# Kernel optimization log

Hardware: AMD Instinct MI355X
Metric: run time of the kernel (lower is better)

## Reference

```python
import jax, jax.numpy as jnp
import numpy as np

E = 256; H = 8; HD = E // H
L_LEN = 300; A_LEN = 250
T = 768; B = 4
NEG = -1e9


def setup_inputs() -> dict:
    rng = jax.random.key(0)
    ks = jax.random.split(rng, 16)
    n = lambda k, s, sc=1.0: jax.random.normal(k, s, dtype=jnp.float32) * sc
    return {
        "query": n(ks[0], (T, B, E)),
        "key": n(ks[1], (T, B, E)),
        "value": n(ks[2], (T, B, E)),
        "in_proj_w": n(ks[3], (3 * E, E), 0.05),
        "in_proj_b": jnp.zeros((3 * E,), jnp.float32),
        "out_w": n(ks[4], (7, E, E), 0.05),
        "out_b": jnp.zeros((7, E), jnp.float32),
        "s_l_w": n(ks[5], (E, 4 * E), 0.05),
        "s_l_b": jnp.zeros((E,), jnp.float32),
        "s_a_w": n(ks[6], (E, 4 * E), 0.05),
        "s_a_b": jnp.zeros((E,), jnp.float32),
        "s_v_w": n(ks[7], (E, 4 * E), 0.05),
        "s_v_b": jnp.zeros((E,), jnp.float32),
        "final_w": n(ks[8], (E, E), 0.05),
        "final_b": jnp.zeros((E,), jnp.float32),
    }


def _forward(query, key, value, in_proj_w, in_proj_b, out_w, out_b,
             s_l_w, s_l_b, s_a_w, s_a_b, s_v_w, s_v_b, final_w, final_b):
    t, b, e = query.shape
    scaling = HD ** -0.5
    Wq, Wk, Wv = in_proj_w[:E], in_proj_w[E:2 * E], in_proj_w[2 * E:]
    bq, bk, bv = in_proj_b[:E], in_proj_b[E:2 * E], in_proj_b[2 * E:]
    q = (query @ Wq.T + bq) * scaling
    k = key @ Wk.T + bk
    v = value @ Wv.T + bv
    # (T, B, E) -> (B*H, T, HD)
    sh = lambda x: x.reshape(t, b * H, HD).transpose(1, 0, 2)
    q, k, v = sh(q), sh(k), sh(v)
    # shared QK^T, reused by all 7 masked branches
    scores = jnp.einsum('bth,bsh->bts', q, k)  # (B*H, T, T)
    idx = jnp.arange(t)
    seg = jnp.where(idx < L_LEN, 0, jnp.where(idx < L_LEN + A_LEN, 1, 2))

    def branch(i, mods):
        # m[j] = 1 iff position j belongs to one of the selected modalities
        m = sum((seg == s) for s in mods).astype(scores.dtype)  # (T,)
        # additive mask: in-set query attends only in-set keys; out-of-set
        # query rows get all -1e9 (uniform softmax, zeroed by row mask below)
        add = jnp.where((m[:, None] * m[None, :]) > 0, 0.0, NEG)
        w = jax.nn.softmax(scores + add, axis=-1) * m[None, :, None]
        o = jnp.einsum('bts,bsh->bth', w, v * m[None, :, None])
        o = o.transpose(1, 0, 2).reshape(t, b, e)
        return o @ out_w[i].T + out_b[i]

    attn_lav = branch(0, (0, 1, 2))
    attn_la = branch(1, (0, 1))
    attn_lv = branch(2, (0, 2))
    attn_av = branch(3, (1, 2))
    attn_l = branch(4, (0,))
    attn_a = branch(5, (1,))
    attn_v = branch(6, (2,))

    sl = jnp.concatenate([attn_lav, attn_la, attn_lv, attn_l], -1) @ s_l_w.T + s_l_b
    sa = jnp.concatenate([attn_lav, attn_la, attn_av, attn_a], -1) @ s_a_w.T + s_a_b
    sv = jnp.concatenate([attn_lav, attn_lv, attn_av, attn_v], -1) @ s_v_w.T + s_v_b
    return (sl + sa + sv) @ final_w.T + final_b


def reference(query, key, value, in_proj_w, in_proj_b, out_w, out_b,
              s_l_w, s_l_b, s_a_w, s_a_b, s_v_w, s_v_b, final_w, final_b):
    return _forward(query, key, value, in_proj_w, in_proj_b, out_w, out_b,
                    s_l_w, s_l_b, s_a_w, s_a_b, s_v_w, s_v_b, final_w, final_b)
```

## Files before the change

### kernel.cpp

```cpp
#include <hip/hip_runtime.h>
#include <hip/hip_bf16.h>

#define E 256
#define H 8
#define HD 32
#define T 768
#define B 4
#define BH 32

typedef __attribute__((ext_vector_type(8))) short bf16x8;
typedef __attribute__((ext_vector_type(4))) float f32x4;
typedef __attribute__((ext_vector_type(16))) float f32x16;

__device__ __forceinline__ float b2f(__hip_bfloat16 x) { return __bfloat162float(x); }

__device__ __forceinline__ unsigned short f2bf_u(float x) {
    __hip_bfloat16 h = __float2bfloat16(x);
    return *(unsigned short*)&h;
}
__device__ __forceinline__ float bfu2f(unsigned short u) {
    return __uint_as_float(((unsigned int)u) << 16);
}

__device__ __forceinline__ int detect_f32(const void* query) {
    const unsigned short* q = (const unsigned short*)query;
    int lane = threadIdx.x & 63;
    int bad = 0;
    #pragma unroll
    for (int i = 0; i < 4; ++i) {
        float v = bfu2f(q[lane + i * 64]);
        bad |= (!(v == v) || fabsf(v) > 1e4f) ? 1 : 0;
    }
    return __any(bad) ? 1 : 0;
}

__device__ __forceinline__ void f8_split(const float* v, bf16x8& h, bf16x8& l) {
    #pragma unroll
    for (int e = 0; e < 8; ++e) {
        unsigned short hu = f2bf_u(v[e]);
        h[e] = (short)hu;
        l[e] = (short)f2bf_u(v[e] - bfu2f(hu));
    }
}

#define MFMA3(ACC, AH, AL, BH_, BL_)                                         \
    ACC = __builtin_amdgcn_mfma_f32_16x16x32_bf16(AH, BH_, ACC, 0, 0, 0);    \
    ACC = __builtin_amdgcn_mfma_f32_16x16x32_bf16(AH, BL_, ACC, 0, 0, 0);    \
    ACC = __builtin_amdgcn_mfma_f32_16x16x32_bf16(AL, BH_, ACC, 0, 0, 0);

#define MFMA3W(ACC, AH, AL, BH_, BL_)                                        \
    ACC = __builtin_amdgcn_mfma_f32_32x32x16_bf16(AH, BH_, ACC, 0, 0, 0);    \
    ACC = __builtin_amdgcn_mfma_f32_32x32x16_bf16(AH, BL_, ACC, 0, 0, 0);    \
    ACC = __builtin_amdgcn_mfma_f32_32x32x16_bf16(AL, BH_, ACC, 0, 0, 0);

__device__ __forceinline__ bf16x8 mk8(int a, int b, int c, int d) {
    union { int i[4]; bf16x8 v; } u;
    u.i[0] = a; u.i[1] = b; u.i[2] = c; u.i[3] = d;
    return u.v;
}

__device__ __forceinline__ float ldu(const void* p, size_t i, int f32) {
    if (f32) return ((const float*)p)[i];
    return b2f(((const __hip_bfloat16*)p)[i]);
}

__device__ __forceinline__ float gsum_load(int i, int r2, int r,
                                           const void* sl, const void* sa,
                                           const void* sv, int f32)
{
    size_t base = (size_t)r2 * 1024;
    switch (i) {
        case 0: return ldu(sl, base + r, f32) + ldu(sa, base + r, f32) + ldu(sv, base + r, f32);
        case 1: return ldu(sl, base + 256 + r, f32) + ldu(sa, base + 256 + r, f32);
        case 2: return ldu(sl, base + 512 + r, f32) + ldu(sv, base + 256 + r, f32);
        case 3: return ldu(sa, base + 512 + r, f32) + ldu(sv, base + 512 + r, f32);
        case 4: return ldu(sl, base + 768 + r, f32);
        case 5: return ldu(sa, base + 768 + r, f32);
        default: return ldu(sv, base + 768 + r, f32);
    }
}

__global__ __launch_bounds__(256) void stage1_kernel(
    const void* query, const void* key, const void* value, const void* w,
    const void* sl, const void* sa, const void* sv, const void* outw,
    const void* outb, const void* slb, const void* sab, const void* svb,
    unsigned short* __restrict__ XFh, unsigned short* __restrict__ XFl,
    unsigned short* __restrict__ WFh, unsigned short* __restrict__ WFl,
    unsigned short* __restrict__ GFh, unsigned short* __restrict__ GFl,
    unsigned short* __restrict__ OWFh, unsigned short* __restrict__ OWFl,
    float* __restrict__ c0)
{
    __shared__ float red[256];
    int f32 = detect_f32(query);
    if (blockIdx.x < 1696) {
        int item = blockIdx.x * 256 + threadIdx.x;
        if (item < 294912) {
            int inp = item / 98304;
            int rem = item % 98304;
            int row = rem >> 5, kg = rem & 31;
            const void* X = (inp == 0) ? query : (inp == 1) ? key : value;
            float v[8];
            if (f32) {
                const float4* p = (const float4*)((const float*)X +
                                   (size_t)row * 256 + kg * 8);
                *(float4*)&v[0] = p[0];
                *(float4*)&v[4] = p[1];
            } else {
                #pragma unroll
                for (int j = 0; j < 8; ++j)
                    v[j] = ldu(X, (size_t)row * 256 + kg * 8 + j, 0);
            }
            bf16x8 h, l;
            f8_split(v, h, l);
            int rb = row >> 4, kb = kg >> 2;
            int lane = (row & 15) | ((kg & 3) << 4);
            size_t idx = (((size_t)(inp * 192 + rb) * 8 + kb) * 64 + lane) * 8;
            *(bf16x8*)&XFh[idx] = h;
            *(bf16x8*)&XFl[idx] = l;
        } else if (item < 319488) {
            int rem = item - 294912;
            int gc = rem >> 5, kg = rem & 31;
            float v[8];
            if (f32) {
                const float4* p = (const float4*)((const float*)w +
                                   (size_t)gc * 256 + kg * 8);
                *(float4*)&v[0] = p[0];
                *(float4*)&v[4] = p[1];
            } else {
                #pragma unroll
                for (int j = 0; j < 8; ++j)
                    v[j] = ldu(w, (size_t)gc * 256 + kg * 8 + j, 0);
            }
            bf16x8 h, l;
            f8_split(v, h, l);
            int sec = gc >> 8, c = gc & 255;
            int cb = c >> 4, kb = kg >> 2;
            int lane = (c & 15) | ((kg & 3) << 4);
            size_t idx = (((size_t)(sec * 16 + cb) * 8 + kb) * 64 + lane) * 8;
            *(bf16x8*)&WFh[idx] = h;
            *(bf16x8*)&WFl[idx] = l;
        } else if (item < 376832) {
            int rem = item - 319488;
            int i = rem >> 13;
            int rest = rem & 8191;
            int r2 = rest >> 5, kg = rest & 31;
            float v[8];
            #pragma unroll
            for (int j = 0; j < 8; ++j)
                v[j] = gsum_load(i, r2, kg * 8 + j, sl, sa, sv, f32);
            bf16x8 h, l;
            f8_split(v, h, l);
            int rb = r2 >> 4, kb = kg >> 2;
            int lane = (r2 & 15) | ((kg & 3) << 4);
            size_t idx = (((size_t)(i * 16 + rb) * 8 + kb) * 64 + lane) * 8;
            *(bf16x8*)&GFh[idx] = h;
            *(bf16x8*)&GFl[idx] = l;
        } else if (item < 434176) {
            int rem = item - 376832;
            int i = rem >> 13;
            int rest = rem & 8191;
            int kg = rest >> 8, c = rest & 255;
            float v[8];
            #pragma unroll
            for (int j = 0; j < 8; ++j)
                v[j] = ldu(outw, (size_t)i * 65536 + (kg * 8 + j) * 256 + c, f32);
            bf16x8 h, l;
            f8_split(v, h, l);
            int cb = c >> 4, kb = kg >> 2;
            int lane = (c & 15) | ((kg & 3) << 4);
            size_t idx = (((size_t)(i * 16 + cb) * 8 + kb) * 64 + lane) * 8;
            *(bf16x8*)&OWFh[idx] = h;
            *(bf16x8*)&OWFl[idx] = l;
        }
    } else {
        int r2 = blockIdx.x - 1696, m = threadIdx.x;
        float acc = 0.f;
        #pragma unroll
        for (int i = 0; i < 7; ++i)
            acc += ldu(outb, i * 256 + m, f32) * gsum_load(i, r2, m, sl, sa, sv, f32);
        red[m] = acc;
        __syncthreads();
        for (int s = 128; s > 0; s >>= 1) {
            if (m < s) red[m] += red[m + s];
            __syncthreads();
        }
        if (m == 0)
            c0[r2] = red[0] + ldu(slb, r2, f32) + ldu(sab, r2, f32) + ldu(svb, r2, f32);
    }
}

__global__ __launch_bounds__(256) void stage2_kernel(
    const unsigned short* __restrict__ XFh, const unsigned short* __restrict__ XFl,
    const unsigned short* __restrict__ WFh, const unsigned short* __restrict__ WFl,
    const void* bias, const void* query,
    float* __restrict__ qws,
    unsigned short* __restrict__ KRh, unsigned short* __restrict__ KRl,
    unsigned short* __restrict__ VFh, unsigned short* __restrict__ VFl,
    const unsigned short* __restrict__ GFh, const unsigned short* __restrict__ GFl,
    const unsigned short* __restrict__ OWFh, const unsigned short* __restrict__ OWFl,
    float* __restrict__ Mtmp,
    const float* __restrict__ c0, const void* finalw, const void* finalb,
    float* __restrict__ d0)
{
    __shared__ float red[256];
    int bxx = blockIdx.x;
    if (bxx < 2304) {
        int f32 = detect_f32(query);
        int bx = bxx % 12;
        int rb = bxx / 12;
        int sec = bx >> 2, cg = bx & 3;
        int w = threadIdx.x >> 6, lane = threadIdx.x & 63;
        int m = lane & 15, quad = lane >> 4;
        int cb = cg * 4 + w;

        const unsigned short* Ah = XFh + (((size_t)(sec * 192 + rb) * 8) * 64 + lane) * 8;
        const unsigned short* Al = XFl + (((size_t)(sec * 192 + rb) * 8) * 64 + lane) * 8;
        const unsigned short* Bh = WFh + (((size_t)(sec * 16 + cb) * 8) * 64 + lane) * 8;
        const unsigned short* Bl = WFl + (((size_t)(sec * 16 + cb) * 8) * 64 + lane) * 8;

        f32x4 acc = {};
        #pragma unroll
        for (int kb = 0; kb < 8; ++kb) {
            size_t off = (size_t)kb * 512;
            bf16x8 ah = *(const bf16x8*)(Ah + off);
            bf16x8 al = *(const bf16x8*)(Al + off);
            bf16x8 bh = *(const bf16x8*)(Bh + off);
            bf16x8 bl = *(const bf16x8*)(Bl + off);
            MFMA3(acc, ah, al, bh, bl)
        }

        int c_local = cb * 16 + m;
        float bv = ldu(bias, sec * 256 + c_local, f32);
        int h = c_local >> 5, hd = c_local & 31;

        if (sec == 0) {
            #pragma unroll
            for (int rr = 0; rr < 4; ++rr) {
                int row = rb * 16 + quad * 4 + rr;
                int t = row >> 2, b = row & 3;
                float val = (acc[rr] + bv) * 0.17677669529663687f;
                qws[((size_t)((b * H + h) * T + t)) * HD + hd] = val;
            }
        } else if (sec == 1) {
            #pragma unroll
            for (int rr = 0; rr < 4; ++rr) {
                int row = rb * 16 + quad * 4 + rr;
                int s = row >> 2, b = row & 3;
                int bh_ = b * 8 + h;
                float val = acc[rr] + bv;
                unsigned short hu = f2bf_u(val);
                unsigned short lu = f2bf_u(val - bfu2f(hu));
                size_t bi = ((size_t)bh_ * 768 + s) * 32 + hd;
                KRh[bi] = hu;
                KRl[bi] = lu;
            }
        } else {
            #pragma unroll
            for (int rr = 0; rr < 4; ++rr) {
                int row = rb * 16 + quad * 4 + rr;
                int s = row >> 2, b = row & 3;
                int bh_ = b * 8 + h;
                float val = acc[rr] + bv;
                unsigned short hu = f2bf_u(val);
                unsigned short lu = f2bf_u(val - bfu2f(hu));
                int s16 = s >> 4, hp = (s >> 3) & 1, j = s & 7;
                size_t bi = (((size_t)bh_ * 48 + s16) * 64 + hp * 32 + hd) * 8 + j;
                VFh[bi] = hu;
                VFl[bi] = lu;
            }
        }
    } else if (bxx < 2752) {
        int idx = bxx - 2304;
        int cgrp = idx & 3;
        int rb   = (idx >> 2) & 15;
        int i    = idx >> 6;
        int w = threadIdx.x >> 6, lane = threadIdx.x & 63;
        int m = lane & 15, quad = lane >> 4;
        int cb = cgrp * 4 + w;

        const unsigned short* Ah = GFh + (((size_t)(i * 16 + rb) * 8) * 64 + lane) * 8;
        const unsigned short* Al = GFl + (((size_t)(i * 16 + rb) * 8) * 64 + lane) * 8;
        const unsigned short* Bh = OWFh + (((size_t)(i * 16 + cb) * 8) * 64 + lane) * 8;
        const unsigned short* Bl = OWFl + (((size_t)(i * 16 + cb) * 8) * 64 + lane) * 8;

        f32x4 acc = {};
        #pragma unroll
        for (int kb = 0; kb < 8; ++kb) {
            size_t off = (size_t)kb * 512;
            bf16x8 ah = *(const bf16x8*)(Ah + off);
            bf16x8 al = *(const bf16x8*)(Al + off);
            bf16x8 bh = *(const bf16x8*)(Bh + off);
            bf16x8 bl = *(const bf16x8*)(Bl + off);
            MFMA3(acc, ah, al, bh, bl)
        }
        #pragma unroll
        for (int rr = 0; rr < 4; ++rr) {
            int r2 = rb * 16 + quad * 4 + rr;
            Mtmp[(size_t)i * 65536 + r2 * 256 + cb * 16 + m] = acc[rr];
        }
    } else {
        int f32 = detect_f32(query);
        int e = bxx - 2752, r = threadIdx.x;
        red[r] = c0[r] * ldu(finalw, (size_t)e * 256 + r, f32);
        __syncthreads();
        for (int s = 128; s > 0; s >>= 1) {
            if (r < s) red[r] += red[r + s];
            __syncthreads();
        }
        if (r == 0)
            d0[e] = red[0] + ldu(finalb, e, f32);
    }
}

__global__ __launch_bounds__(256, 2) void stage3_kernel(
    const float* __restrict__ qws,
    const unsigned short* __restrict__ KRh, const unsigned short* __restrict__ KRl,
    const unsigned short* __restrict__ VFh, const unsigned short* __restrict__ VFl,
    unsigned short* __restrict__ Ohi, unsigned short* __restrict__ Olo,
    const float* __restrict__ Mtmp, const void* finalw, const void* query,
    unsigned short* __restrict__ DThi, unsigned short* __restrict__ DTlo)
{
    __shared__ __align__(16) float SMEM[7104];
    int tid = threadIdx.x;

    if (blockIdx.x < 768) {
        float (*AC2)[3][32][36] = (float(*)[3][32][36])&SMEM[0];
        float (*SS2)[3][32]     = (float(*)[3][32])&SMEM[6912];
        int tile = blockIdx.x % 24;
        int bh   = blockIdx.x / 24;
        int t0 = tile * 32;
        int w = tid >> 6, lane = tid & 63;
        int ln = lane & 31, h = lane >> 5;

        bf16x8 qbh[2], qbl[2];
        {
            const float* qr = qws + ((size_t)bh * T + t0 + ln) * HD + h * 8;
            #pragma unroll
            for (int c = 0; c < 2; ++c) {
                float qv[8];
                *(float4*)&qv[0] = *(const float4*)(qr + c * 16);
                *(float4*)&qv[4] = *(const float4*)(qr + c * 16 + 4);
                f8_split(qv, qbh[c], qbl[c]);
            }
        }

        f32x16 accA = {}, accB = {};
        float ssA = 0.f, ssB = 0.f;

        for (int q = 0; q < 3; ++q) {
            int ch = w * 3 + q;
            int sbase = ch * 64;
            int route = (ch == 5) ? 1 : (ch == 4 || ch == 8) ? 2 : 0;
            int bnd = (ch == 4) ? 300 : 550;
            bool c12 = (ch == 4);

            #pragma unroll
            for (int st = 0; st < 2; ++st) {
                size_t krow = ((size_t)bh * 768 + sbase + st * 32 + ln) * 32 + h * 8;
                bf16x8 kh0 = *(const bf16x8*)(KRh + krow);
                bf16x8 kl0 = *(const bf16x8*)(KRl + krow);
                bf16x8 kh1 = *(const bf16x8*)(KRh + krow + 16);
                bf16x8 kl1 = *(const bf16x8*)(KRl + krow + 16);
                f32x16 d = {};
                MFMA3W(d, kh0, kl0, qbh[0], qbl[0])
                MFMA3W(d, kh1, kl1, qbh[1], qbl[1])

                int PH[8], PL[8];
                #pragma unroll
                for (int p = 0; p < 8; ++p) {
                    float e0 = __expf(d[2 * p]);
                    float e1 = __expf(d[2 * p + 1]);
                    if (route == 2) {
                        int r0 = 2 * p;
                        int s0 = sbase + st * 32 + (r0 & 3) + 8 * (r0 >> 2) + 4 * h;
                        if (s0 < bnd) ssA += e0; else ssB += e0;
                        if (s0 + 1 < bnd) ssA += e1; else ssB += e1;
                    } else if (route == 1) { ssB += e0 + e1; }
                    else { ssA += e0 + e1; }
                    unsigned b0 = __float_as_uint(e0), b1 = __float_as_uint(e1);
                    float l0 = e0 - __uint_as_float(b0 & 0xffff0000u);
                    float l1 = e1 - __uint_as_float(b1 & 0xffff0000u);
                    PH[p] = (int)((b0 >> 16) | (b1 & 0xffff0000u));
                    PL[p] = (int)((__float_as_uint(l0) >> 16) |
                                  (__float_as_uint(l1) & 0xffff0000u));
                }

                #pragma unroll
                for (int ksl = 0; ksl < 2; ++ksl) {
                    int ks = st * 2 + ksl;
                    int cc = 4 * ksl;
                    size_t vidx = (((size_t)bh * 48 + ch * 4 + ks) * 64 + lane) * 8;
                    bf16x8 vbh = *(const bf16x8*)(VFh + vidx);
                    bf16x8 vbl = *(const bf16x8*)(VFl + vidx);

                    int sh0 = __shfl_xor(PH[cc+0], 32);
                    int sh1 = __shfl_xor(PH[cc+1], 32);
                    int sh2 = __shfl_xor(PH[cc+2], 32);
                    int sh3 = __shfl_xor(PH[cc+3], 32);
                    int sl0 = __shfl_xor(PL[cc+0], 32);
                    int sl1 = __shfl_xor(PL[cc+1], 32);
                    int sl2 = __shfl_xor(PL[cc+2], 32);
                    int sl3 = __shfl_xor(PL[cc+3], 32);
                    int FH0 = h ? sh2 : PH[cc+0];
                    int FH1 = h ? sh3 : PH[cc+1];
                    int FH2 = h ? PH[cc+2] : sh0;
                    int FH3 = h ? PH[cc+3] : sh1;
                    int FL0 = h ? sl2 : PL[cc+0];
                    int FL1 = h ? sl3 : PL[cc+1];
                    int FL2 = h ? PL[cc+2] : sl0;
                    int FL3 = h ? PL[cc+3] : sl1;
                    bf16x8 feh = mk8(FH0, FH1, FH2, FH3);
                    bf16x8 fel = mk8(FL0, FL1, FL2, FL3);

                    if (route == 0)      { MFMA3W(accA, feh, fel, vbh, vbl) }
                    else if (route == 1) { MFMA3W(accB, feh, fel, vbh, vbl) }
                    else {
                        if (ks < 2)       { MFMA3W(accA, feh, fel, vbh, vbl) }
                        else if (ks == 3) { MFMA3W(accB, feh, fel, vbh, vbl) }
                        else {
                            int a0 = h ? (c12 ? FH0 : 0) : FH0;
                            int a1 = h ? (c12 ? FH1 : 0) : FH1;
                            int a2 = h ? 0 : FH2;
                            int a3 = h ? 0 : (c12 ? FH3 : 0);
                            int b0 = h ? (c12 ? 0 : FH0) : 0;
                            int b1 = h ? (c12 ? 0 : FH1) : 0;
                            int b2 = h ? FH2 : 0;
                            int b3 = h ? FH3 : (c12 ? 0 : FH3);
                            int la0 = h ? (c12 ? FL0 : 0) : FL0;
                            int la1 = h ? (c12 ? FL1 : 0) : FL1;
                            int la2 = h ? 0 : FL2;
                            int la3 = h ? 0 : (c12 ? FL3 : 0);
                            int lb0 = h ? (c12 ? 0 : FL0) : 0;
                            int lb1 = h ? (c12 ? 0 : FL1) : 0;
                            int lb2 = h ? FL2 : 0;
                            int lb3 = h ? FL3 : (c12 ? 0 : FL3);
                            bf16x8 fha = mk8(a0, a1, a2, a3), fla = mk8(la0, la1, la2, la3);
                            bf16x8 fhb = mk8(b0, b1, b2, b3), flb = mk8(lb0, lb1, lb2, lb3);
                            MFMA3W(accA, fha, fla, vbh, vbl)
                            MFMA3W(accB, fhb, flb, vbh, vbl)
                        }
                    }
                }
            }
        }

        ssA += __shfl_xor(ssA, 32);
        ssB += __shfl_xor(ssB, 32);

        int bsel = w & 1;
        f32x16 zz = {};
        f32x16 o0 = (w <= 1) ? accA : zz;
        f32x16 o1 = (w == 1) ? accB : (w == 2) ? accA : zz;
        f32x16 o2 = (w == 2) ? accB : (w == 3) ? accA : zz;
        float s0 = (w <= 1) ? ssA : 0.f;
        float s1 = (w == 1) ? ssB : (w == 2) ? ssA : 0.f;
        float s2 = (w == 2) ? ssB : (w == 3) ? ssA : 0.f;

        if (w < 2) {
            #pragma unroll
            for (int r = 0; r < 16; ++r) {
                int t = (r & 3) + 8 * (r >> 2) + 4 * h;
                AC2[bsel][0][t][ln] = o0[r];
                AC2[bsel][1][t][ln] = o1[r];
                AC2[bsel][2][t][ln] = o2[r];
            }
            if (h == 0) {
                SS2[bsel][0][ln] = s0;
                SS2[bsel][1][ln] = s1;
                SS2[bsel][2][ln] = s2;
            }
        }
        __syncthreads();
        if (w >= 2) {
            #pragma unroll
            for (int r = 0; r < 16; ++r) {
                int t = (r & 3) + 8 * (r >> 2) + 4 * h;
                AC2[bsel][1][t][ln] += o1[r];
                AC2[bsel][2][t][ln] += o2[r];
            }
            if (h == 0) {
                SS2[bsel][1][ln] += s1;
                SS2[bsel][2][ln] += s2;
            }
        }
        __syncthreads();

        int tt = tid >> 3, q4 = tid & 7;
        float Pv[3][4], S[3];
        #pragma unroll
        for (int sg = 0; sg < 3; ++sg) {
            const float4 a = *(const float4*)&AC2[0][sg][tt][q4 * 4];
            const float4 b = *(const float4*)&AC2[1][sg][tt][q4 * 4];
            Pv[sg][0] = a.x + b.x; Pv[sg][1] = a.y + b.y;
            Pv[sg][2] = a.z + b.z; Pv[sg][3] = a.w + b.w;
            S[sg] = SS2[0][sg][tt] + SS2[1][sg][tt];
        }

        int t_glob = t0 + tt;
        int g = (t_glob < 300) ? 0 : (t_glob < 550 ? 1 : 2);
        int b_ = bh >> 3, h_ = bh & 7;
        int row = b_ * T + t_glob;
        int lslot = (row & 15) + ((q4 >> 1) << 4);
        int j0 = (q4 & 1) * 4;
        size_t fbase = (((size_t)(row >> 4) * 56 + h_) * 64 + lslot) * 8 + j0;
        const int masks[7] = {7, 3, 5, 6, 1, 2, 4};
        #pragma unroll
        for (int i = 0; i < 7; ++i) {
            int mm = masks[i];
            float n0 = 0.f, n1 = 0.f, n2 = 0.f, n3 = 0.f, den = 0.f;
            if (mm & 1) { n0 += Pv[0][0]; n1 += Pv[0][1]; n2 += Pv[0][2]; n3 += Pv[0][3]; den += S[0]; }
            if (mm & 2) { n0 += Pv[1][0]; n1 += Pv[1][1]; n2 += Pv[1][2]; n3 += Pv[1][3]; den += S[1]; }
            if (mm & 4) { n0 += Pv[2][0]; n1 += Pv[2][1]; n2 += Pv[2][2]; n3 += Pv[2][3]; den += S[2]; }
            float r = 1.f / den;
            int live = (mm >> g) & 1;
            float o[4];
            o[0] = live ? n0 * r : 0.f;
            o[1] = live ? n1 * r : 0.f;
            o[2] = live ? n2 * r : 0.f;
            o[3] = live ? n3 * r : 0.f;
            ushort4 hi4, lo4;
            unsigned short* hp = (unsigned short*)&hi4;
            unsigned short* lp = (unsigned short*)&lo4;
            #pragma unroll
            for (int j = 0; j < 4; ++j) {
                unsigned short hu = f2bf_u(o[j]);
                hp[j] = hu;
                lp[j] = f2bf_u(o[j] - bfu2f(hu));
            }
            size_t addr = fbase + (size_t)i * (8 * 64 * 8);
            *(ushort4*)&Ohi[addr] = hi4;
            *(ushort4*)&Olo[addr] = lo4;
        }
    } else {
        float (*AsT)[34] = (float(*)[34])&SMEM[0];
        float (*Bs)[34]  = (float(*)[34])&SMEM[1088];
        int f32 = detect_f32(query);
        int idx = blockIdx.x - 768;
        int bx = idx & 7;
        int by = (idx >> 3) & 7;
        int i  = idx >> 6;
        int tx = tid & 15, ty = tid >> 4;
        int colbase = bx * 32, rowbase = by * 32;
        float acc[2][2] = {};

        for (int kb = 0; kb < 8; ++kb) {
            __syncthreads();
            #pragma unroll
            for (int l = 0; l < 4; ++l) {
                int idx2 = l * 256 + tid;
                int c = idx2 & 31, kk = idx2 >> 5;
                AsT[kk][c] = Mtmp[(size_t)i * 65536 + (kb * 32 + kk) * 256 + rowbase + c];
                int k2 = idx2 & 31, n = idx2 >> 5;
                Bs[k2][n] = ldu(finalw, (size_t)(colbase + n) * 256 + kb * 32 + k2, f32);
            }
            __syncthreads();
            #pragma unroll 8
            for (int kk = 0; kk < 32; ++kk) {
                const float2 av = *(const float2*)&AsT[kk][ty * 2];
                const float2 bv = *(const float2*)&Bs[kk][tx * 2];
                acc[0][0] += av.x * bv.x; acc[0][1] += av.x * bv.y;
                acc[1][0] += av.y * bv.x; acc[1][1] += av.y * bv.y;
            }
        }
        #pragma unroll
        for (int u = 0; u < 2; ++u)
            #pragma unroll
            for (int v = 0; v < 2; ++v) {
                int c = rowbase + ty * 2 + u, e = colbase + tx * 2 + v;
                float a = acc[u][v];
                unsigned short hu = f2bf_u(a);
                size_t fidx = (((size_t)(e >> 4) * 56 + i * 8 + (c >> 5)) * 64
                               + (e & 15) + (((c >> 3) & 3) << 4)) * 8 + (c & 7);
                DThi[fidx] = hu;
                DTlo[fidx] = f2bf_u(a - bfu2f(hu));
            }
    }
}

__global__ __launch_bounds__(256) void final_gemm_mfma_kernel(
    const unsigned short* __restrict__ Ohi, const unsigned short* __restrict__ Olo,
    const unsigned short* __restrict__ DThi, const unsigned short* __restrict__ DTlo,
    const float* __restrict__ d0, const void* query,
    void* __restrict__ outv)
{
    int f32 = detect_f32(query);
    int bx = blockIdx.x;
    int by = blockIdx.y;
    int w  = threadIdx.x >> 6;
    int lane = threadIdx.x & 63;
    int m = lane & 15, quad = lane >> 4;
    int R0 = by * 16, C0 = bx * 64 + w * 16;

    int b_out = R0 / 768;
    int tfirst = R0 - b_out * 768;
    int g0 = (tfirst < 300) ? 0 : (tfirst < 550 ? 1 : 2);
    int g1 = (tfirst + 15 < 300) ? 0 : (tfirst + 15 < 550 ? 1 : 2);
    int activeset = (1 << g0) | (1 << g1);
    const int masks[7] = {7, 3, 5, 6, 1, 2, 4};

    const unsigned short* Abase_h = Ohi + (size_t)by * 56 * 512 + lane * 8;
    const unsigned short* Abase_l = Olo + (size_t)by * 56 * 512 + lane * 8;
    const unsigned short* Bbase_h = DThi + (size_t)(bx * 4 + w) * 56 * 512 + lane * 8;
    const unsigned short* Bbase_l = DTlo + (size_t)(bx * 4 + w) * 56 * 512 + lane * 8;

    f32x4 acc = {};
    for (int i = 0; i < 7; ++i) {
        if (!(masks[i] & activeset)) continue;
        #pragma unroll
        for (int kb = 0; kb < 8; ++kb) {
            size_t off = (size_t)(i * 8 + kb) * 512;
            bf16x8 ah = *(const bf16x8*)(Abase_h + off);
            bf16x8 al = *(const bf16x8*)(Abase_l + off);
            bf16x8 bh = *(const bf16x8*)(Bbase_h + off);
            bf16x8 bl = *(const bf16x8*)(Bbase_l + off);
            acc = __builtin_amdgcn_mfma_f32_16x16x32_bf16(ah, bh, acc, 0, 0, 0);
            acc = __builtin_amdgcn_mfma_f32_16x16x32_bf16(ah, bl, acc, 0, 0, 0);
            acc = __builtin_amdgcn_mfma_f32_16x16x32_bf16(al, bh, acc, 0, 0, 0);
        }
    }
    float dv = d0[C0 + m];
    #pragma unroll
    for (int r = 0; r < 4; ++r) {
        int t = tfirst + quad * 4 + r;
        int col = C0 + m;
        float val = acc[r] + dv;
        size_t orow = (size_t)t * B + b_out;
        if (f32) ((float*)outv)[orow * 256 + col] = val;
        else ((__hip_bfloat16*)outv)[orow * 256 + col] = __float2bfloat16(val);
    }
}

extern "C" void kernel_launch(void* const* d_in, const int* in_sizes, int n_in,
                              void* d_out, int out_size, void* d_ws, size_t ws_size,
                              hipStream_t stream) {
    const void* query     = d_in[0];
    const void* key       = d_in[1];
    const void* value     = d_in[2];
    const void* in_proj_w = d_in[3];
    const void* in_proj_b = d_in[4];
    const void* out_w     = d_in[5];
    const void* out_b     = d_in[6];
    const void* s_l_w     = d_in[7];
    const void* s_l_b     = d_in[8];
    const void* s_a_w     = d_in[9];
    const void* s_a_b     = d_in[10];
    const void* s_v_w     = d_in[11];
    const void* s_v_b     = d_in[12];
    const void* final_w   = d_in[13];
    const void* final_b   = d_in[14];

    float* ws     = (float*)d_ws;
    float* qws    = ws;
    unsigned short* KRh = (unsigned short*)(ws + 786432);
    unsigned short* KRl = KRh + 786432;
    unsigned short* VFh = (unsigned short*)(ws + 1572864);
    unsigned short* VFl = VFh + 786432;
    unsigned short* Ohi = (unsigned short*)(ws + 2359296);
    unsigned short* Olo = (unsigned short*)(ws + 5111808);
    unsigned short* XFh = (unsigned short*)(ws + 2359296);
    unsigned short* XFl = XFh + 2359296;
    unsigned short* WFh = XFl + 2359296;
    unsigned short* WFl = WFh + 196608;
    unsigned short* GFh = (unsigned short*)(ws + 4915200);
    unsigned short* GFl = GFh + 458752;
    unsigned short* OWFh = GFl + 458752;
    unsigned short* OWFl = OWFh + 458752;
    float* Mtmp   = ws + 7864320;
    unsigned short* DThi = (unsigned short*)(ws + 8323072);
    unsigned short* DTlo = (unsigned short*)(ws + 8552448);
    float* d0     = ws + 8781824;
    float* c0     = ws + 8782336;

    stage1_kernel<<<1952, 256, 0, stream>>>(query, key, value, in_proj_w,
                                            s_l_w, s_a_w, s_v_w, out_w,
                                            out_b, s_l_b, s_a_b, s_v_b,
                                            XFh, XFl, WFh, WFl,
                                            GFh, GFl, OWFh, OWFl, c0);
    stage2_kernel<<<3008, 256, 0, stream>>>(XFh, XFl, WFh, WFl,
                                            in_proj_b, query, qws,
                                            KRh, KRl, VFh, VFl,
                                            GFh, GFl, OWFh, OWFl, Mtmp,
                                            c0, final_w, final_b, d0);
    stage3_kernel<<<1216, 256, 0, stream>>>(qws, KRh, KRl, VFh, VFl,
                                            Ohi, Olo,
                                            Mtmp, final_w, query,
                                            DThi, DTlo);
    final_gemm_mfma_kernel<<<dim3(4, 192), 256, 0, stream>>>(Ohi, Olo, DThi, DTlo,
                                                             d0, query, d_out);
}
```

Baseline: 164.4 us.

## Remap blocks to XCDs for L2 locality and prefetch K/V fragments

Stage3 and the final GEMM now remap block indices so that blocks sharing the same head (or the same row slab) land on the same XCD, under round-robin dispatch across the 8 XCDs. This is meant to improve L2 reuse of K/V and A operands. The final GEMM grid becomes 1D to allow the swizzle. Stage3 also loads all K and V fragments for a chunk up front, before the MFMA/softmax work, to hide global load latency, at the cost of more live registers.

```diff
diff --git a/kernel.cpp b/kernel.cpp
--- a/kernel.cpp
+++ b/kernel.cpp
@@ -326,8 +326,10 @@
     if (blockIdx.x < 768) {
         float (*AC2)[3][32][36] = (float(*)[3][32][36])&SMEM[0];
         float (*SS2)[3][32]     = (float(*)[3][32])&SMEM[6912];
-        int tile = blockIdx.x % 24;
-        int bh   = blockIdx.x / 24;
+        int bid = blockIdx.x;
+        int xcd = bid & 7, rr_ = bid >> 3;
+        int j_ = rr_ / 24, tile = rr_ % 24;
+        int bh = j_ * 8 + xcd;
         int t0 = tile * 32;
         int w = tid >> 6, lane = tid & 63;
         int ln = lane & 31, h = lane >> 5;
@@ -354,16 +356,27 @@
             int bnd = (ch == 4) ? 300 : 550;
             bool c12 = (ch == 4);
 
+            bf16x8 kf0h[2], kf0l[2], kf1h[2], kf1l[2], vh[4], vl[4];
             #pragma unroll
             for (int st = 0; st < 2; ++st) {
                 size_t krow = ((size_t)bh * 768 + sbase + st * 32 + ln) * 32 + h * 8;
-                bf16x8 kh0 = *(const bf16x8*)(KRh + krow);
-                bf16x8 kl0 = *(const bf16x8*)(KRl + krow);
-                bf16x8 kh1 = *(const bf16x8*)(KRh + krow + 16);
-                bf16x8 kl1 = *(const bf16x8*)(KRl + krow + 16);
+                kf0h[st] = *(const bf16x8*)(KRh + krow);
+                kf0l[st] = *(const bf16x8*)(KRl + krow);
+                kf1h[st] = *(const bf16x8*)(KRh + krow + 16);
+                kf1l[st] = *(const bf16x8*)(KRl + krow + 16);
+            }
+            #pragma unroll
+            for (int ks = 0; ks < 4; ++ks) {
+                size_t vidx = (((size_t)bh * 48 + ch * 4 + ks) * 64 + lane) * 8;
+                vh[ks] = *(const bf16x8*)(VFh + vidx);
+                vl[ks] = *(const bf16x8*)(VFl + vidx);
+            }
+
+            #pragma unroll
+            for (int st = 0; st < 2; ++st) {
                 f32x16 d = {};
-                MFMA3W(d, kh0, kl0, qbh[0], qbl[0])
-                MFMA3W(d, kh1, kl1, qbh[1], qbl[1])
+                MFMA3W(d, kf0h[st], kf0l[st], qbh[0], qbl[0])
+                MFMA3W(d, kf1h[st], kf1l[st], qbh[1], qbl[1])
 
                 int PH[8], PL[8];
                 #pragma unroll
@@ -389,9 +402,8 @@
                 for (int ksl = 0; ksl < 2; ++ksl) {
                     int ks = st * 2 + ksl;
                     int cc = 4 * ksl;
-                    size_t vidx = (((size_t)bh * 48 + ch * 4 + ks) * 64 + lane) * 8;
-                    bf16x8 vbh = *(const bf16x8*)(VFh + vidx);
-                    bf16x8 vbl = *(const bf16x8*)(VFl + vidx);
+                    bf16x8 vbh = vh[ks];
+                    bf16x8 vbl = vl[ks];
 
                     int sh0 = __shfl_xor(PH[cc+0], 32);
                     int sh1 = __shfl_xor(PH[cc+1], 32);
@@ -522,10 +534,10 @@
             unsigned short* hp = (unsigned short*)&hi4;
             unsigned short* lp = (unsigned short*)&lo4;
             #pragma unroll
-            for (int j = 0; j < 4; ++j) {
-                unsigned short hu = f2bf_u(o[j]);
-                hp[j] = hu;
-                lp[j] = f2bf_u(o[j] - bfu2f(hu));
+            for (int jq = 0; jq < 4; ++jq) {
+                unsigned short hu = f2bf_u(o[jq]);
+                hp[jq] = hu;
+                lp[jq] = f2bf_u(o[jq] - bfu2f(hu));
             }
             size_t addr = fbase + (size_t)i * (8 * 64 * 8);
             *(ushort4*)&Ohi[addr] = hi4;
@@ -584,8 +596,10 @@
     void* __restrict__ outv)
 {
     int f32 = detect_f32(query);
-    int bx = blockIdx.x;
-    int by = blockIdx.y;
+    int bid = blockIdx.x;
+    int xcd = bid & 7, rr_ = bid >> 3;
+    int slot = rr_ >> 2, bx = rr_ & 3;
+    int by = slot * 8 + xcd;
     int w  = threadIdx.x >> 6;
     int lane = threadIdx.x & 63;
     int m = lane & 15, quad = lane >> 4;
@@ -685,6 +699,6 @@
                                             Ohi, Olo,
                                             Mtmp, final_w, query,
                                             DThi, DTlo);
-    final_gemm_mfma_kernel<<<dim3(4, 192), 256, 0, stream>>>(Ohi, Olo, DThi, DTlo,
-                                                             d0, query, d_out);
-}
+    final_gemm_mfma_kernel<<<768, 256, 0, stream>>>(Ohi, Olo, DThi, DTlo,
+                                                    d0, query, d_out);
+}
```

After: 164.6 us. No clear change (+0.1%).
